# Performance work log

Hardware: AMD Instinct MI355X
Metric: run time of the kernel (lower is better)

The kernel has to match this reference:

```python
import jax, jax.numpy as jnp
import numpy as np

FACTOR = 5

def setup_inputs() -> dict:
    key = jax.random.key(0)
    kq, kk, kv, ki = jax.random.split(key, 4)
    B, L, H, D = 8, 2048, 8, 64
    u = FACTOR * int(np.ceil(np.log(L)))  # sample_k == n_top == 40
    return {
        "queries": jax.random.normal(kq, (B, L, H, D), dtype=jnp.float32),
        "keys": jax.random.normal(kk, (B, L, H, D), dtype=jnp.float32),
        "values": jax.random.normal(kv, (B, L, H, D), dtype=jnp.float32),
        "index_sample": jax.random.randint(ki, (L, u), 0, L, dtype=jnp.int32),
    }

def reference(queries, keys, values, index_sample):
    B, L, H, D = queries.shape
    # faithful to torch .view(B, H, -1, D) on contiguous tensors (a reshape, not a transpose)
    q = queries.reshape(B, H, L, D)
    k = keys.reshape(B, H, L, D)
    v = values.reshape(B, H, L, D)
    u = FACTOR * int(np.ceil(np.log(L)))  # U_part == u
    # --- _prob_QK: sample keys per query, score, pick top-u queries ---
    K_sample = k[:, :, index_sample, :]                      # [B,H,L,u,D] gather over L_K
    QK_sample = jnp.einsum('bhld,bhlsd->bhls', q, K_sample)  # [B,H,L,u]
    M = QK_sample.max(axis=-1) - QK_sample.sum(axis=-1) / L  # sparsity measure [B,H,L]
    M_top = jax.lax.top_k(M, u)[1]                           # [B,H,u] indices of active queries
    Q_reduce = jnp.take_along_axis(q, M_top[..., None], axis=2)  # [B,H,u,D]
    scores = jnp.einsum('bhud,bhld->bhul', Q_reduce, k)      # [B,H,u,L]
    scale = 1.0 / float(np.sqrt(D))
    attn = jax.nn.softmax(scores * scale, axis=-1)           # dropout is identity in eval
    context = jnp.einsum('bhul,bhld->bhud', attn, v)         # [B,H,u,D]
    return context, attn
```

## Files before the change

### kernel.cpp

```cpp
#include <hip/hip_runtime.h>
#include <math.h>

#define LSEQ 2048
#define DDIM 64
#define UU   40
#define NBH  64
#define CTX_ELEMS (NBH*UU*DDIM)

__global__ __launch_bounds__(256, 4) void k12_sample_m(
    const float* __restrict__ q, const float* __restrict__ k,
    const int* __restrict__ idxs, float* __restrict__ M) {
  int b = blockIdx.x;
  int bh = b & 63;
  int ltile = b >> 6;
  int t = threadIdx.x;
  int g = t >> 2;
  int sub = t & 3;
  int l = ltile * 64 + g;

  const float4* qr = (const float4*)(q + (size_t)(bh * LSEQ + l) * DDIM);
  float4 qv[4];
#pragma unroll
  for (int m = 0; m < 4; ++m) qv[m] = qr[4 * m + sub];

  const float* kbase = k + (size_t)bh * LSEQ * DDIM;
  const int4* ir = (const int4*)(idxs + l * UU);

  float mx = -INFINITY, sm = 0.f;
#pragma unroll 1
  for (int s4 = 0; s4 < UU / 4; ++s4) {
    int4 jv = ir[s4];
    const float4* k0 = (const float4*)(kbase + (size_t)jv.x * DDIM);
    const float4* k1 = (const float4*)(kbase + (size_t)jv.y * DDIM);
    const float4* k2 = (const float4*)(kbase + (size_t)jv.z * DDIM);
    const float4* k3 = (const float4*)(kbase + (size_t)jv.w * DDIM);
    float d0 = 0.f, d1 = 0.f, d2 = 0.f, d3 = 0.f;
#pragma unroll
    for (int m = 0; m < 4; ++m) {
      float4 a = k0[4 * m + sub];
      float4 x = qv[m];
      d0 += x.x * a.x + x.y * a.y + x.z * a.z + x.w * a.w;
    }
#pragma unroll
    for (int m = 0; m < 4; ++m) {
      float4 a = k1[4 * m + sub];
      float4 x = qv[m];
      d1 += x.x * a.x + x.y * a.y + x.z * a.z + x.w * a.w;
    }
#pragma unroll
    for (int m = 0; m < 4; ++m) {
      float4 a = k2[4 * m + sub];
      float4 x = qv[m];
      d2 += x.x * a.x + x.y * a.y + x.z * a.z + x.w * a.w;
    }
#pragma unroll
    for (int m = 0; m < 4; ++m) {
      float4 a = k3[4 * m + sub];
      float4 x = qv[m];
      d3 += x.x * a.x + x.y * a.y + x.z * a.z + x.w * a.w;
    }
    d0 += __shfl_xor(d0, 1, 64); d0 += __shfl_xor(d0, 2, 64);
    d1 += __shfl_xor(d1, 1, 64); d1 += __shfl_xor(d1, 2, 64);
    d2 += __shfl_xor(d2, 1, 64); d2 += __shfl_xor(d2, 2, 64);
    d3 += __shfl_xor(d3, 1, 64); d3 += __shfl_xor(d3, 2, 64);
    mx = fmaxf(fmaxf(fmaxf(mx, d0), fmaxf(d1, d2)), d3);
    sm += (d0 + d1) + (d2 + d3);
  }
  if (sub == 0) M[bh * LSEQ + l] = mx - sm * (1.0f / (float)LSEQ);
}

__global__ __launch_bounds__(256) void k3_topk(const float* __restrict__ M,
                                               int* __restrict__ Mtop) {
  int bh = blockIdx.x;
  int t = threadIdx.x;
  int w = t >> 6;
  int lane = t & 63;
  float v[8];
#pragma unroll
  for (int j = 0; j < 8; ++j) v[j] = M[bh * LSEQ + t + 256 * j];
  __shared__ float swv[4];
  __shared__ int   swi[4];
  __shared__ int   win;
  for (int it = 0; it < UU; ++it) {
    float bv = -INFINITY; int bi = 0x7fffffff;
#pragma unroll
    for (int j = 0; j < 8; ++j) {
      if (v[j] > bv) { bv = v[j]; bi = t + 256 * j; }
    }
#pragma unroll
    for (int off = 32; off > 0; off >>= 1) {
      float ov = __shfl_xor(bv, off, 64);
      int   oi = __shfl_xor(bi, off, 64);
      if (ov > bv || (ov == bv && oi < bi)) { bv = ov; bi = oi; }
    }
    if (lane == 0) { swv[w] = bv; swi[w] = bi; }
    __syncthreads();
    if (t == 0) {
      float fv = swv[0]; int fi = swi[0];
#pragma unroll
      for (int j = 1; j < 4; ++j) {
        if (swv[j] > fv || (swv[j] == fv && swi[j] < fi)) { fv = swv[j]; fi = swi[j]; }
      }
      Mtop[bh * UU + it] = fi;
      win = fi;
    }
    __syncthreads();
    int wi = win;
    if ((wi & 255) == t) v[wi >> 8] = -INFINITY;
  }
}

__global__ __launch_bounds__(256, 4) void k45_scores_softmax(
    const float* __restrict__ q, const float* __restrict__ k,
    const int* __restrict__ Mtop, float* __restrict__ attn,
    float* __restrict__ ctx) {
  __shared__ float sct[4 * LSEQ];
  int b = blockIdx.x;
  int bh = b & 63;
  int u0 = (b >> 6) * 4;
  int t = threadIdx.x;
  int g = t >> 2;
  int sub = t & 3;

  ctx[b * 256 + t] = 0.f;

  float4 qv[4][4];
#pragma unroll
  for (int u = 0; u < 4; ++u) {
    int qi = Mtop[bh * UU + u0 + u];
    const float4* qr = (const float4*)(q + (size_t)(bh * LSEQ + qi) * DDIM);
#pragma unroll
    for (int m = 0; m < 4; ++m) qv[u][m] = qr[4 * m + sub];
  }

  const float* kb = k + (size_t)bh * LSEQ * DDIM;
#pragma unroll 1
  for (int p = 0; p < 32; ++p) {
    int l = p * 64 + g;
    const float4* kr = (const float4*)(kb + (size_t)l * DDIM);
    float4 ks[4];
#pragma unroll
    for (int m = 0; m < 4; ++m) ks[m] = kr[4 * m + sub];
    float d[4];
#pragma unroll
    for (int u = 0; u < 4; ++u) {
      float s = 0.f;
#pragma unroll
      for (int m = 0; m < 4; ++m) {
        float4 x = qv[u][m], a = ks[m];
        s += x.x * a.x + x.y * a.y + x.z * a.z + x.w * a.w;
      }
      s += __shfl_xor(s, 1, 64);
      s += __shfl_xor(s, 2, 64);
      d[u] = s * 0.125f;
    }
    if (sub == 0) {
#pragma unroll
      for (int u = 0; u < 4; ++u) sct[u * LSEQ + l] = d[u];
    }
  }
  __syncthreads();

  int w = t >> 6, lane = t & 63;
  float* row = sct + w * LSEQ;
  float vv[32];
  float mx = -INFINITY;
#pragma unroll
  for (int j = 0; j < 32; ++j) { vv[j] = row[lane + 64 * j]; mx = fmaxf(mx, vv[j]); }
#pragma unroll
  for (int off = 32; off > 0; off >>= 1) mx = fmaxf(mx, __shfl_xor(mx, off, 64));
  float sm = 0.f;
#pragma unroll
  for (int j = 0; j < 32; ++j) { vv[j] = __expf(vv[j] - mx); sm += vv[j]; }
#pragma unroll
  for (int off = 32; off > 0; off >>= 1) sm += __shfl_xor(sm, off, 64);
  float inv = 1.0f / sm;
  float* ap = attn + (size_t)(bh * UU + u0 + w) * LSEQ;
#pragma unroll
  for (int j = 0; j < 32; ++j) ap[lane + 64 * j] = vv[j] * inv;
}

__global__ __launch_bounds__(256) void k7_context(
    const float* __restrict__ attn, const float* __restrict__ v,
    float* __restrict__ ctx) {
  __shared__ float vt[256 * DDIM];
  int b = blockIdx.x;
  int bh = b & 63;
  int l0 = (b >> 6) * 256;
  int t = threadIdx.x;

  const float4* src = (const float4*)(v + ((size_t)bh * LSEQ + l0) * DDIM);
  float4* dst = (float4*)vt;
#pragma unroll
  for (int i = 0; i < 16; ++i) dst[t + 256 * i] = src[t + 256 * i];
  __syncthreads();

  int w = t >> 6;
  int d = t & 63;
  const float* ab = attn + ((size_t)bh * UU + w * 10) * LSEQ + l0;
  float acc[10];
#pragma unroll
  for (int u = 0; u < 10; ++u) acc[u] = 0.f;
#pragma unroll 1
  for (int l4 = 0; l4 < 64; ++l4) {
    int l = l4 * 4;
    float4 av[10];
#pragma unroll
    for (int u = 0; u < 10; ++u)
      av[u] = *(const float4*)(ab + (size_t)u * LSEQ + l);
#pragma unroll
    for (int i = 0; i < 4; ++i) {
      float vvv = vt[(l + i) * DDIM + d];
#pragma unroll
      for (int u = 0; u < 10; ++u)
        acc[u] = fmaf(((const float*)&av[u])[i], vvv, acc[u]);
    }
  }
#pragma unroll
  for (int u = 0; u < 10; ++u)
    atomicAdd(&ctx[((size_t)bh * UU + w * 10 + u) * DDIM + d], acc[u]);
}

extern "C" void kernel_launch(void* const* d_in, const int* in_sizes, int n_in,
                              void* d_out, int out_size, void* d_ws, size_t ws_size,
                              hipStream_t stream) {
  const float* q   = (const float*)d_in[0];
  const float* k   = (const float*)d_in[1];
  const float* v   = (const float*)d_in[2];
  const int*   idx = (const int*)d_in[3];

  float* ctx  = (float*)d_out;
  float* attn = (float*)d_out + CTX_ELEMS;

  float* M    = (float*)d_ws;
  int*   Mtop = (int*)(M + NBH * LSEQ);

  k12_sample_m<<<NBH * 32, 256, 0, stream>>>(q, k, idx, M);
  k3_topk<<<NBH, 256, 0, stream>>>(M, Mtop);
  k45_scores_softmax<<<NBH * 10, 256, 0, stream>>>(q, k, Mtop, attn, ctx);
  k7_context<<<NBH * 8, 256, 0, stream>>>(attn, v, ctx);
}
```

Baseline: 305.1 us.

## Bucket sampled key indices by chunk and score samples from LDS-staged key tiles

A new pre-pass groups each query's sampled key indices by 256-row chunk. The sampling kernel then stages one chunk of K per block in shared memory and computes partial max/sum per query from LDS instead of doing random global gathers. Partial results go to a scratch area that aliases the attn output, and top-k merges the 8 partials per query. This trades scattered global K reads for a full sweep of Q per chunk block, 8x more partial-result traffic and an extra launch.

```diff
diff --git a/kernel.cpp b/kernel.cpp
--- a/kernel.cpp
+++ b/kernel.cpp
@@ -5,71 +5,87 @@
 #define DDIM 64
 #define UU   40
 #define NBH  64
+#define NCHUNK 8
+#define CROWS  256
 #define CTX_ELEMS (NBH*UU*DDIM)
 
-__global__ __launch_bounds__(256, 4) void k12_sample_m(
+__global__ __launch_bounds__(256) void k0_sort(
+    const int* __restrict__ idxs, int* __restrict__ sidx, int* __restrict__ soff) {
+  int l = blockIdx.x * 4 + (threadIdx.x >> 6);
+  int lane = threadIdx.x & 63;
+  int v = 0, c = NCHUNK;
+  if (lane < UU) { v = idxs[l * UU + lane]; c = v >> 8; }
+  unsigned long long lower = (1ull << lane) - 1ull;
+  int base = 0;
+#pragma unroll
+  for (int cc = 0; cc < NCHUNK; ++cc) {
+    unsigned long long m = __ballot(c == cc);
+    if (c == cc) {
+      int rank = __popcll(m & lower);
+      sidx[l * UU + base + rank] = v;
+    }
+    int cnt = __popcll(m);
+    if (lane == cc) soff[l * NCHUNK + cc] = (base << 8) | cnt;
+    base += cnt;
+  }
+}
+
+__global__ __launch_bounds__(256, 2) void k12_gather(
     const float* __restrict__ q, const float* __restrict__ k,
-    const int* __restrict__ idxs, float* __restrict__ M) {
+    const int* __restrict__ sidx, const int* __restrict__ soff,
+    float2* __restrict__ Mpart) {
+  __shared__ float kt[CROWS * DDIM];
   int b = blockIdx.x;
   int bh = b & 63;
-  int ltile = b >> 6;
-  int t = threadIdx.x;
-  int g = t >> 2;
-  int sub = t & 3;
-  int l = ltile * 64 + g;
-
-  const float4* qr = (const float4*)(q + (size_t)(bh * LSEQ + l) * DDIM);
-  float4 qv[4];
-#pragma unroll
-  for (int m = 0; m < 4; ++m) qv[m] = qr[4 * m + sub];
-
-  const float* kbase = k + (size_t)bh * LSEQ * DDIM;
-  const int4* ir = (const int4*)(idxs + l * UU);
-
-  float mx = -INFINITY, sm = 0.f;
-#pragma unroll 1
-  for (int s4 = 0; s4 < UU / 4; ++s4) {
-    int4 jv = ir[s4];
-    const float4* k0 = (const float4*)(kbase + (size_t)jv.x * DDIM);
-    const float4* k1 = (const float4*)(kbase + (size_t)jv.y * DDIM);
-    const float4* k2 = (const float4*)(kbase + (size_t)jv.z * DDIM);
-    const float4* k3 = (const float4*)(kbase + (size_t)jv.w * DDIM);
-    float d0 = 0.f, d1 = 0.f, d2 = 0.f, d3 = 0.f;
-#pragma unroll
-    for (int m = 0; m < 4; ++m) {
-      float4 a = k0[4 * m + sub];
-      float4 x = qv[m];
-      d0 += x.x * a.x + x.y * a.y + x.z * a.z + x.w * a.w;
-    }
-#pragma unroll
-    for (int m = 0; m < 4; ++m) {
-      float4 a = k1[4 * m + sub];
-      float4 x = qv[m];
-      d1 += x.x * a.x + x.y * a.y + x.z * a.z + x.w * a.w;
-    }
-#pragma unroll
-    for (int m = 0; m < 4; ++m) {
-      float4 a = k2[4 * m + sub];
-      float4 x = qv[m];
-      d2 += x.x * a.x + x.y * a.y + x.z * a.z + x.w * a.w;
-    }
-#pragma unroll
-    for (int m = 0; m < 4; ++m) {
-      float4 a = k3[4 * m + sub];
-      float4 x = qv[m];
-      d3 += x.x * a.x + x.y * a.y + x.z * a.z + x.w * a.w;
-    }
-    d0 += __shfl_xor(d0, 1, 64); d0 += __shfl_xor(d0, 2, 64);
-    d1 += __shfl_xor(d1, 1, 64); d1 += __shfl_xor(d1, 2, 64);
-    d2 += __shfl_xor(d2, 1, 64); d2 += __shfl_xor(d2, 2, 64);
-    d3 += __shfl_xor(d3, 1, 64); d3 += __shfl_xor(d3, 2, 64);
-    mx = fmaxf(fmaxf(fmaxf(mx, d0), fmaxf(d1, d2)), d3);
-    sm += (d0 + d1) + (d2 + d3);
-  }
-  if (sub == 0) M[bh * LSEQ + l] = mx - sm * (1.0f / (float)LSEQ);
-}
-
-__global__ __launch_bounds__(256) void k3_topk(const float* __restrict__ M,
+  int c  = b >> 6;
+  int t  = threadIdx.x;
+
+  const float4* src = (const float4*)(k + ((size_t)bh * LSEQ + c * CROWS) * DDIM);
+  float4* dst = (float4*)kt;
+#pragma unroll
+  for (int i = 0; i < 16; ++i) dst[t + 256 * i] = src[t + 256 * i];
+  __syncthreads();
+
+  int w = t >> 6, lane = t & 63;
+  int slot = lane >> 3, sub = lane & 7;
+
+  for (int l = w; l < LSEQ; l += 4) {
+    int oc   = soff[l * NCHUNK + c];
+    int cnt  = oc & 255;
+    int base = oc >> 8;
+    const float4* qr = (const float4*)(q + ((size_t)bh * LSEQ + l) * DDIM);
+    float4 qa = qr[sub];
+    float4 qb = qr[sub + 8];
+    float mx = -INFINITY, sm = 0.f;
+    for (int it = 0; it < cnt; it += 8) {
+      int sj = it + slot;
+      float d = 0.f;
+      if (sj < cnt) {
+        int row = sidx[l * UU + base + sj] & (CROWS - 1);
+        const float4* kr = (const float4*)(kt + row * DDIM);
+        float4 a = kr[sub], bb = kr[sub + 8];
+        d = qa.x * a.x + qa.y * a.y + qa.z * a.z + qa.w * a.w
+          + qb.x * bb.x + qb.y * bb.y + qb.z * bb.z + qb.w * bb.w;
+      }
+      d += __shfl_xor(d, 1, 64);
+      d += __shfl_xor(d, 2, 64);
+      d += __shfl_xor(d, 4, 64);
+      float dm = (sj < cnt) ? d : -INFINITY;
+      float ds = (sj < cnt) ? d : 0.f;
+      dm = fmaxf(dm, __shfl_xor(dm, 8, 64));
+      dm = fmaxf(dm, __shfl_xor(dm, 16, 64));
+      dm = fmaxf(dm, __shfl_xor(dm, 32, 64));
+      ds += __shfl_xor(ds, 8, 64);
+      ds += __shfl_xor(ds, 16, 64);
+      ds += __shfl_xor(ds, 32, 64);
+      mx = fmaxf(mx, dm);
+      sm += ds;
+    }
+    if (lane == 0) Mpart[((size_t)bh * NCHUNK + c) * LSEQ + l] = make_float2(mx, sm);
+  }
+}
+
+__global__ __launch_bounds__(256) void k3_topk(const float2* __restrict__ Mp,
                                                int* __restrict__ Mtop) {
   int bh = blockIdx.x;
   int t = threadIdx.x;
@@ -77,7 +93,17 @@
   int lane = t & 63;
   float v[8];
 #pragma unroll
-  for (int j = 0; j < 8; ++j) v[j] = M[bh * LSEQ + t + 256 * j];
+  for (int j = 0; j < 8; ++j) {
+    int l = t + 256 * j;
+    float mxv = -INFINITY, smv = 0.f;
+#pragma unroll
+    for (int c = 0; c < NCHUNK; ++c) {
+      float2 p = Mp[((size_t)bh * NCHUNK + c) * LSEQ + l];
+      mxv = fmaxf(mxv, p.x);
+      smv += p.y;
+    }
+    v[j] = mxv - smv * (1.0f / (float)LSEQ);
+  }
   __shared__ float swv[4];
   __shared__ int   swi[4];
   __shared__ int   win;
@@ -106,7 +132,9 @@
     }
     __syncthreads();
     int wi = win;
-    if ((wi & 255) == t) v[wi >> 8] = -INFINITY;
+#pragma unroll
+    for (int j = 0; j < 8; ++j)
+      if (wi == t + 256 * j) v[j] = -INFINITY;
   }
 }
 
@@ -231,12 +259,15 @@
 
   float* ctx  = (float*)d_out;
   float* attn = (float*)d_out + CTX_ELEMS;
-
-  float* M    = (float*)d_ws;
-  int*   Mtop = (int*)(M + NBH * LSEQ);
-
-  k12_sample_m<<<NBH * 32, 256, 0, stream>>>(q, k, idx, M);
-  k3_topk<<<NBH, 256, 0, stream>>>(M, Mtop);
+  float2* Mpart = (float2*)attn;
+
+  int* sidx = (int*)d_ws;
+  int* soff = sidx + LSEQ * UU;
+  int* Mtop = soff + LSEQ * NCHUNK;
+
+  k0_sort<<<LSEQ / 4, 256, 0, stream>>>(idx, sidx, soff);
+  k12_gather<<<NBH * NCHUNK, 256, 0, stream>>>(q, k, sidx, soff, Mpart);
+  k3_topk<<<NBH, 256, 0, stream>>>(Mpart, Mtop);
   k45_scores_softmax<<<NBH * 10, 256, 0, stream>>>(q, k, Mtop, attn, ctx);
   k7_context<<<NBH * 8, 256, 0, stream>>>(attn, v, ctx);
 }
```

Result: slower. 734.2 us (+140.6%).
